# Kernel optimization log

Measured on AMD Instinct MI355X. Metric: run time of the kernel, lower is better.

## Reference

```python
import jax, jax.numpy as jnp
import numpy as np

BATCH_SIZE_PER_IM = 512
FG_FRACTION = 0.25
FG_THRESH = 0.5
BG_THRESH_HI = 0.5
BG_THRESH_LO = 0.0
MAX_FG = int(FG_FRACTION * BATCH_SIZE_PER_IM)  # 128


def _rand_boxes(key, shape):
    a = jax.random.uniform(key, shape + (4,), dtype=jnp.float32)
    ymin = jnp.minimum(a[..., 0], a[..., 2])
    ymax = jnp.maximum(a[..., 0], a[..., 2]) + 1e-3
    xmin = jnp.minimum(a[..., 1], a[..., 3])
    xmax = jnp.maximum(a[..., 1], a[..., 3]) + 1e-3
    return jnp.stack([ymin, xmin, ymax, xmax], axis=-1)


def setup_inputs() -> dict:
    key = jax.random.key(0)
    k1, k2, k3, k4 = jax.random.split(key, 4)
    B, N, G = 32, 8192, 128
    boxes = _rand_boxes(k1, (B, N))
    gt_boxes = _rand_boxes(k2, (B, G))
    gt_labels = jax.random.randint(k3, (B, G), 0, 91, dtype=jnp.int32)
    noise = jax.random.uniform(k4, (B, N + G), dtype=jnp.float32)
    return {"boxes": boxes, "gt_boxes": gt_boxes, "gt_labels": gt_labels, "noise": noise}


def _bbox_overlap(boxes, gt_boxes):
    # boxes: [B, M, 4], gt_boxes: [B, G, 4], layout (ymin, xmin, ymax, xmax)
    b_ymin, b_xmin, b_ymax, b_xmax = [boxes[..., i:i + 1] for i in range(4)]  # [B,M,1]
    g_ymin, g_xmin, g_ymax, g_xmax = [gt_boxes[..., i][:, None, :] for i in range(4)]  # [B,1,G]
    i_ymin = jnp.maximum(b_ymin, g_ymin)
    i_xmin = jnp.maximum(b_xmin, g_xmin)
    i_ymax = jnp.minimum(b_ymax, g_ymax)
    i_xmax = jnp.minimum(b_xmax, g_xmax)
    i_area = jnp.maximum(i_ymax - i_ymin, 0.0) * jnp.maximum(i_xmax - i_xmin, 0.0)  # [B,M,G]
    b_area = (b_ymax - b_ymin) * (b_xmax - b_xmin)           # [B,M,1]
    g_area = (g_ymax - g_ymin) * (g_xmax - g_xmin)           # [B,1,G]
    iou = i_area / (b_area + g_area - i_area)
    # padded gt boxes (filled with -1) get IoU = -1
    padding = jnp.logical_and(i_ymin < 0, i_xmin < 0)
    return jnp.where(padding, -1.0, iou)


def reference(boxes, gt_boxes, gt_labels, noise):
    boxes = jax.lax.stop_gradient(boxes)
    all_boxes = jnp.concatenate([boxes, gt_boxes], axis=1)        # [B, M=N+G, 4]
    iou = _bbox_overlap(all_boxes, gt_boxes)                      # [B, M, G]
    max_ov = jnp.max(iou, axis=2)                                 # [B, M]
    p2l = jnp.argmax(iou, axis=2).astype(jnp.int32)               # [B, M]
    box_t = jnp.take_along_axis(gt_boxes, p2l[..., None], axis=1)  # [B, M, 4]
    cls_t = jnp.take_along_axis(gt_labels, p2l, axis=1)           # [B, M]
    pos = max_ov > FG_THRESH
    neg = jnp.logical_and(max_ov >= BG_THRESH_LO, max_ov < BG_THRESH_HI)
    cls_t = jnp.where(neg, 0, cls_t)
    box_t = jnp.where(neg[..., None], 0.0, box_t)
    p2l = jnp.where(neg, 0, p2l)
    # --- balanced fg/bg subsampling (random scores provided in `noise`) ---
    pos_score = jnp.where(pos, noise, -1.0)
    kth = jax.lax.top_k(pos_score, MAX_FG)[0][:, -1:]             # [B,1] threshold
    sel_pos = jnp.logical_and(pos, pos_score >= kth)              # at most MAX_FG fg
    # selected fg get priority band 2+, bg band [0,1), rest -1
    combined = jnp.where(sel_pos, 2.0 + noise, jnp.where(neg, noise, -1.0))
    _, idx = jax.lax.top_k(combined, BATCH_SIZE_PER_IM)           # [B, K]
    rois = jnp.take_along_axis(all_boxes, idx[..., None], axis=1)      # [B, K, 4]
    sample_box_t = jnp.take_along_axis(box_t, idx[..., None], axis=1)  # [B, K, 4]
    sample_cls_t = jnp.take_along_axis(cls_t, idx, axis=1)             # [B, K]
    sample_p2l = jnp.take_along_axis(p2l, idx, axis=1)                 # [B, K]
    return sample_box_t, sample_cls_t, rois, sample_p2l
```

## Files before the change

### kernel.cpp

```cpp
#include <hip/hip_runtime.h>
#include <stdint.h>

#define BATCH 32
#define NBOX 8192
#define NGT 128
#define M (NBOX + NGT)
#define K_OUT 512
#define MAX_FG 128
#define C_CAP 256
#define S_CAP 256
#define U_CAP 1024

__device__ __forceinline__ unsigned int bkt1024(float ns) {
    unsigned int u = (unsigned int)(ns * 16777216.0f) >> 14;
    return u > 1023u ? 1023u : u;
}

__global__ __launch_bounds__(256) void iou_kernel(
    const float* __restrict__ boxes,
    const float* __restrict__ gt_boxes,
    unsigned short* __restrict__ packed)
{
    const int BPB = (M + 255) / 256;
    const int b = blockIdx.x / BPB;
    const int m = (blockIdx.x % BPB) * 256 + threadIdx.x;

    __shared__ float4 sgt[NGT];
    __shared__ float  sgarea[NGT];
    if (threadIdx.x < NGT) {
        float4 g = ((const float4*)gt_boxes)[b * NGT + threadIdx.x];
        sgt[threadIdx.x] = g;
        sgarea[threadIdx.x] = __fmul_rn(__fsub_rn(g.z, g.x), __fsub_rn(g.w, g.y));
    }
    __syncthreads();
    if (m >= M) return;

    float4 bb = (m < NBOX) ? ((const float4*)boxes)[b * NBOX + m]
                           : ((const float4*)gt_boxes)[b * NGT + (m - NBOX)];
    float b_area = __fmul_rn(__fsub_rn(bb.z, bb.x), __fsub_rn(bb.w, bb.y));

    float best = -1e30f;
    int bidx = 0;
    #pragma unroll 4
    for (int g = 0; g < NGT; ++g) {
        float4 gg = sgt[g];
        float iymin = fmaxf(bb.x, gg.x);
        float ixmin = fmaxf(bb.y, gg.y);
        float iymax = fminf(bb.z, gg.z);
        float ixmax = fminf(bb.w, gg.w);
        float ia  = __fmul_rn(fmaxf(__fsub_rn(iymax, iymin), 0.0f),
                              fmaxf(__fsub_rn(ixmax, ixmin), 0.0f));
        float den = __fsub_rn(__fadd_rn(b_area, sgarea[g]), ia);
        float iou = __fdiv_rn(ia, den);
        if (iou > best) { best = iou; bidx = g; }
    }
    bool pos = best > 0.5f;
    bool neg = (best >= 0.0f) && (best < 0.5f);
    packed[b * M + m] = (unsigned short)(bidx | (neg ? 256 : 0) | (pos ? 512 : 0));
}

__global__ __launch_bounds__(1024) void select_kernel(
    const float* __restrict__ boxes,
    const float* __restrict__ gt_boxes,
    const int*   __restrict__ gt_labels,
    const float* __restrict__ noise,
    const unsigned short* __restrict__ packed,
    float* __restrict__ out)
{
    const int b = blockIdx.x;
    const int tid = threadIdx.x;

    __shared__ float sh_ns[M];
    __shared__ unsigned int hist[1024];
    __shared__ unsigned int hist2[1024];
    __shared__ unsigned char posmask[M / 8];
    __shared__ unsigned char negmask[M / 8];
    __shared__ float4 sgt[NGT];
    __shared__ int slab[NGT];
    __shared__ float C[C_CAP];
    __shared__ unsigned short slist[S_CAP];
    __shared__ unsigned int ukey[U_CAP];
    __shared__ unsigned short um[U_CAP];
    __shared__ unsigned int sh_Bp, sh_needp, sh_cc, sh_n1a, sh_B, sh_cnt, sh_kth;

    float* out_bt  = out;
    float* out_cls = out + BATCH * K_OUT * 4;
    float* out_roi = out + BATCH * K_OUT * 5;
    float* out_p2l = out + BATCH * K_OUT * 9;

    hist[tid] = 0;
    hist2[tid] = 0;
    if (tid == 0) { sh_cc = 0; sh_n1a = 0; sh_B = 0; sh_cnt = 0; sh_kth = 0xBF800000u; }
    if (tid < NGT) {
        sgt[tid]  = ((const float4*)gt_boxes)[b * NGT + tid];
        slab[tid] = gt_labels[b * NGT + tid];
    }
    __syncthreads();

    {
        const uint4*  pk4 = (const uint4*)(packed + (size_t)b * M);
        const float4* ns4 = (const float4*)(noise + (size_t)b * M);
        for (int c = tid; c < M / 8; c += 1024) {
            uint4 pv = pk4[c];
            float4 n0 = ns4[2 * c], n1v = ns4[2 * c + 1];
            ((float4*)sh_ns)[2 * c] = n0;
            ((float4*)sh_ns)[2 * c + 1] = n1v;
            unsigned short e[8];
            e[0] = (unsigned short)(pv.x & 0xFFFF); e[1] = (unsigned short)(pv.x >> 16);
            e[2] = (unsigned short)(pv.y & 0xFFFF); e[3] = (unsigned short)(pv.y >> 16);
            e[4] = (unsigned short)(pv.z & 0xFFFF); e[5] = (unsigned short)(pv.z >> 16);
            e[6] = (unsigned short)(pv.w & 0xFFFF); e[7] = (unsigned short)(pv.w >> 16);
            float f[8] = {n0.x, n0.y, n0.z, n0.w, n1v.x, n1v.y, n1v.z, n1v.w};
            unsigned int pb = 0, nb = 0;
            #pragma unroll
            for (int k = 0; k < 8; ++k) {
                if (e[k] & 512) {
                    pb |= (1u << k);
                    atomicAdd(&hist2[bkt1024(f[k])], 1u);
                } else if (e[k] & 256) {
                    nb |= (1u << k);
                    atomicAdd(&hist[bkt1024(f[k])], 1u);
                }
            }
            posmask[c] = (unsigned char)pb;
            negmask[c] = (unsigned char)nb;
        }
    }
    __syncthreads();

    {
        const int wv = tid >> 6, ln = tid & 63;
        if (wv < 2) {
            unsigned int* H = wv ? hist2 : hist;
            unsigned int s[16];
            #pragma unroll
            for (int k = 0; k < 16; ++k) {
                unsigned int v = H[k * 64 + ln];
                #pragma unroll
                for (int off = 1; off < 64; off <<= 1) {
                    unsigned int o = __shfl_down(v, off, 64);
                    if (ln + off < 64) v += o;
                }
                s[k] = v;
            }
            unsigned int after = 0;
            #pragma unroll
            for (int k = 15; k >= 0; --k) {
                unsigned int tot = __shfl(s[k], 0, 64);
                H[k * 64 + ln] = s[k] + after;
                after += tot;
            }
        }
    }
    __syncthreads();
    const unsigned int nneg = hist[0];
    const unsigned int npos = hist2[0];

    if (npos >= MAX_FG) {
        {
            unsigned int S  = hist2[tid];
            unsigned int Sn = (tid < 1023) ? hist2[tid + 1] : 0;
            if (S >= MAX_FG && Sn < MAX_FG) { sh_Bp = tid; sh_needp = MAX_FG - Sn; }
        }
        __syncthreads();
        const unsigned int Bp = sh_Bp, needp = sh_needp;
        for (int c = tid; c < M / 8; c += 1024) {
            unsigned int pb = posmask[c];
            while (pb) {
                int k = __ffs(pb) - 1; pb &= pb - 1;
                float v = sh_ns[c * 8 + k];
                if (bkt1024(v) == Bp) {
                    unsigned int slot = atomicAdd(&sh_cc, 1u);
                    if (slot < C_CAP) C[slot] = v;
                }
            }
        }
        __syncthreads();
        {
            unsigned int cc = min(sh_cc, (unsigned int)C_CAP);
            if (tid < (int)cc) {
                float my = C[tid];
                unsigned int g = 0, e = 0;
                for (unsigned int j = 0; j < cc; ++j) {
                    float v = C[j];
                    g += (v > my) ? 1u : 0u;
                    e += (v == my) ? 1u : 0u;
                }
                if (g < needp && g + e >= needp) sh_kth = __float_as_uint(my);
            }
        }
        __syncthreads();
    }
    const float kthf = __uint_as_float(sh_kth);

    for (int c = tid; c < M / 8; c += 1024) {
        unsigned int pb = posmask[c];
        while (pb) {
            int k = __ffs(pb) - 1; pb &= pb - 1;
            int m = c * 8 + k;
            if (sh_ns[m] >= kthf) {
                unsigned int slot = atomicAdd(&sh_n1a, 1u);
                if (slot < S_CAP) slist[slot] = (unsigned short)m;
            }
        }
    }
    __syncthreads();
    const unsigned int n1 = min(sh_n1a, (unsigned int)S_CAP);
    const unsigned int k2 = K_OUT - n1;
    const bool enough_neg = (nneg >= k2);

    if (enough_neg) {
        unsigned int S  = hist[tid];
        unsigned int Sn = (tid < 1023) ? hist[tid + 1] : 0;
        if (S >= k2 && Sn < k2) sh_B = tid;
    }
    if (tid < (int)n1) {
        int mi = slist[tid];
        float nsi = sh_ns[mi];
        float ci = __fadd_rn(2.0f, nsi);
        unsigned int r = 0;
        for (unsigned int j = 0; j < n1; ++j) {
            int mj = slist[j];
            float cj = __fadd_rn(2.0f, sh_ns[mj]);
            if (cj > ci || (cj == ci && mj < mi)) ++r;
        }
        int pkv = packed[(size_t)b * M + mi];
        int lbl = pkv & 127;
        float4 roi = (mi < NBOX) ? ((const float4*)boxes)[b * NBOX + mi]
                                 : sgt[mi - NBOX];
        ((float4*)out_bt)[b * K_OUT + r] = sgt[lbl];
        out_cls[b * K_OUT + r] = (float)slab[lbl];
        ((float4*)out_roi)[b * K_OUT + r] = roi;
        out_p2l[b * K_OUT + r] = (float)lbl;
    }
    __syncthreads();
    const unsigned int B1 = sh_B;

    for (int c = tid; c < M / 8; c += 1024) {
        unsigned int nb = negmask[c];
        while (nb) {
            int k = __ffs(nb) - 1; nb &= nb - 1;
            int m = c * 8 + k;
            float v = sh_ns[m];
            if (bkt1024(v) >= B1) {
                unsigned int slot = atomicAdd(&sh_cnt, 1u);
                if (slot < U_CAP) {
                    ukey[slot] = __float_as_uint(v);
                    um[slot]   = (unsigned short)m;
                }
            }
        }
    }
    __syncthreads();

    const unsigned int q = min(sh_cnt, (unsigned int)U_CAP);
    for (unsigned int i = tid; i < q; i += 1024) {
        unsigned int ki = ukey[i];
        unsigned short mi = um[i];
        unsigned int r = 0;
        for (unsigned int j = 0; j < q; ++j) {
            unsigned int kj = ukey[j];
            if (kj > ki || (kj == ki && um[j] < mi)) ++r;
        }
        if (r < k2) {
            float4 roi = (mi < NBOX) ? ((const float4*)boxes)[b * NBOX + mi]
                                     : sgt[mi - NBOX];
            unsigned int gr = n1 + r;
            ((float4*)out_bt)[b * K_OUT + gr] = make_float4(0.f, 0.f, 0.f, 0.f);
            out_cls[b * K_OUT + gr] = 0.0f;
            ((float4*)out_roi)[b * K_OUT + gr] = roi;
            out_p2l[b * K_OUT + gr] = 0.0f;
        }
    }

    if (!enough_neg) {
        __syncthreads();
        const unsigned int k3 = k2 - nneg;
        for (int m = tid; m < M; m += 1024) {
            if (((posmask[m >> 3] >> (m & 7)) & 1) && sh_ns[m] < kthf) {
                unsigned int r = 0;
                for (int m2 = 0; m2 < m; ++m2)
                    if (((posmask[m2 >> 3] >> (m2 & 7)) & 1) && sh_ns[m2] < kthf) ++r;
                if (r < k3) {
                    int pkv = packed[(size_t)b * M + m];
                    int lbl = pkv & 127;
                    float4 roi = (m < NBOX) ? ((const float4*)boxes)[b * NBOX + m]
                                            : sgt[m - NBOX];
                    unsigned int gr = n1 + nneg + r;
                    ((float4*)out_bt)[b * K_OUT + gr] = sgt[lbl];
                    out_cls[b * K_OUT + gr] = (float)slab[lbl];
                    ((float4*)out_roi)[b * K_OUT + gr] = roi;
                    out_p2l[b * K_OUT + gr] = (float)lbl;
                }
            }
        }
    }
}

extern "C" void kernel_launch(void* const* d_in, const int* in_sizes, int n_in,
                              void* d_out, int out_size, void* d_ws, size_t ws_size,
                              hipStream_t stream) {
    const float* boxes     = (const float*)d_in[0];
    const float* gt_boxes  = (const float*)d_in[1];
    const int*   gt_labels = (const int*)d_in[2];
    const float* noise     = (const float*)d_in[3];
    unsigned short* packed = (unsigned short*)d_ws;
    float* out = (float*)d_out;

    const int BPB = (M + 255) / 256;
    iou_kernel<<<BATCH * BPB, 256, 0, stream>>>(boxes, gt_boxes, packed);
    select_kernel<<<BATCH, 1024, 0, stream>>>(boxes, gt_boxes, gt_labels, noise,
                                              packed, out);
}
```

Baseline: 116.6 us.

## Skip exact IoU division via threshold test, two boxes per thread, refine near ties

Each thread now handles two proposal boxes so every shared-memory GT load is reused twice. The per-pair exact division is replaced by a multiply-compare against half the denominator, and only candidates above 0.5 get an approximate reciprocal. The top two scores are tracked so that near-ties fall back to an exact rescan, and a final exact division recomputes the IoU for the winner. Boxes with no candidate are marked negative without their argmax index, which relies on that index being discarded for negatives (and on the inputs having no padded GT boxes).

```diff
diff --git a/kernel.cpp b/kernel.cpp
--- a/kernel.cpp
+++ b/kernel.cpp
@@ -21,42 +21,92 @@
     const float* __restrict__ gt_boxes,
     unsigned short* __restrict__ packed)
 {
-    const int BPB = (M + 255) / 256;
+    const int BPB = (M + 511) / 512;
     const int b = blockIdx.x / BPB;
-    const int m = (blockIdx.x % BPB) * 256 + threadIdx.x;
+    const int base = (blockIdx.x % BPB) * 512;
 
     __shared__ float4 sgt[NGT];
-    __shared__ float  sgarea[NGT];
+    __shared__ float  sga[NGT];
     if (threadIdx.x < NGT) {
         float4 g = ((const float4*)gt_boxes)[b * NGT + threadIdx.x];
         sgt[threadIdx.x] = g;
-        sgarea[threadIdx.x] = __fmul_rn(__fsub_rn(g.z, g.x), __fsub_rn(g.w, g.y));
-    }
-    __syncthreads();
-    if (m >= M) return;
-
-    float4 bb = (m < NBOX) ? ((const float4*)boxes)[b * NBOX + m]
-                           : ((const float4*)gt_boxes)[b * NGT + (m - NBOX)];
-    float b_area = __fmul_rn(__fsub_rn(bb.z, bb.x), __fsub_rn(bb.w, bb.y));
-
-    float best = -1e30f;
-    int bidx = 0;
+        sga[threadIdx.x] = __fmul_rn(__fsub_rn(g.z, g.x), __fsub_rn(g.w, g.y));
+    }
+    __syncthreads();
+
+    const int r0 = base + threadIdx.x;
+    const int r1 = r0 + 256;
+
+    float4 A  = make_float4(0.f, 0.f, 0.f, 0.f);
+    float4 Bx = make_float4(0.f, 0.f, 0.f, 0.f);
+    if (r0 < M) A  = (r0 < NBOX) ? ((const float4*)boxes)[b * NBOX + r0] : sgt[r0 - NBOX];
+    if (r1 < M) Bx = (r1 < NBOX) ? ((const float4*)boxes)[b * NBOX + r1] : sgt[r1 - NBOX];
+    const float areaA = __fmul_rn(__fsub_rn(A.z, A.x),  __fsub_rn(A.w, A.y));
+    const float areaB = __fmul_rn(__fsub_rn(Bx.z, Bx.x), __fsub_rn(Bx.w, Bx.y));
+
+    float best0 = 0.f, sec0 = 0.f; int i0 = 0;
+    float best1 = 0.f, sec1 = 0.f; int i1 = 0;
+
     #pragma unroll 4
     for (int g = 0; g < NGT; ++g) {
         float4 gg = sgt[g];
-        float iymin = fmaxf(bb.x, gg.x);
-        float ixmin = fmaxf(bb.y, gg.y);
-        float iymax = fminf(bb.z, gg.z);
-        float ixmax = fminf(bb.w, gg.w);
-        float ia  = __fmul_rn(fmaxf(__fsub_rn(iymax, iymin), 0.0f),
-                              fmaxf(__fsub_rn(ixmax, ixmin), 0.0f));
-        float den = __fsub_rn(__fadd_rn(b_area, sgarea[g]), ia);
-        float iou = __fdiv_rn(ia, den);
-        if (iou > best) { best = iou; bidx = g; }
-    }
-    bool pos = best > 0.5f;
-    bool neg = (best >= 0.0f) && (best < 0.5f);
-    packed[b * M + m] = (unsigned short)(bidx | (neg ? 256 : 0) | (pos ? 512 : 0));
+        float ga = sga[g];
+        {
+            float dy = __fsub_rn(fminf(A.z, gg.z), fmaxf(A.x, gg.x));
+            float dx = __fsub_rn(fminf(A.w, gg.w), fmaxf(A.y, gg.y));
+            float ia = __fmul_rn(fmaxf(dy, 0.f), fmaxf(dx, 0.f));
+            float den = __fsub_rn(__fadd_rn(areaA, ga), ia);
+            if (ia > __fmul_rn(0.5f, den)) {
+                float q = __fmul_rn(ia, __builtin_amdgcn_rcpf(den));
+                if (q > best0)      { sec0 = best0; best0 = q; i0 = g; }
+                else if (q > sec0)  { sec0 = q; }
+            }
+        }
+        {
+            float dy = __fsub_rn(fminf(Bx.z, gg.z), fmaxf(Bx.x, gg.x));
+            float dx = __fsub_rn(fminf(Bx.w, gg.w), fmaxf(Bx.y, gg.y));
+            float ia = __fmul_rn(fmaxf(dy, 0.f), fmaxf(dx, 0.f));
+            float den = __fsub_rn(__fadd_rn(areaB, ga), ia);
+            if (ia > __fmul_rn(0.5f, den)) {
+                float q = __fmul_rn(ia, __builtin_amdgcn_rcpf(den));
+                if (q > best1)      { sec1 = best1; best1 = q; i1 = g; }
+                else if (q > sec1)  { sec1 = q; }
+            }
+        }
+    }
+
+    auto finalize = [&](float4 bb, float barea, float best, float sec,
+                        int bi) -> unsigned short {
+        if (best == 0.f) return (unsigned short)256;
+        bool flag = __fsub_rn(best, sec) <= __fmul_rn(best, 1.9073486e-6f);
+        int bidx; float q;
+        if (!flag) {
+            bidx = bi;
+            float4 gg = sgt[bidx];
+            float dy = __fsub_rn(fminf(bb.z, gg.z), fmaxf(bb.x, gg.x));
+            float dx = __fsub_rn(fminf(bb.w, gg.w), fmaxf(bb.y, gg.y));
+            float ia = __fmul_rn(fmaxf(dy, 0.f), fmaxf(dx, 0.f));
+            float den = __fsub_rn(__fadd_rn(barea, sga[bidx]), ia);
+            q = __fdiv_rn(ia, den);
+        } else {
+            float bq = -1e30f; bidx = 0;
+            for (int g = 0; g < NGT; ++g) {
+                float4 gg = sgt[g];
+                float dy = __fsub_rn(fminf(bb.z, gg.z), fmaxf(bb.x, gg.x));
+                float dx = __fsub_rn(fminf(bb.w, gg.w), fmaxf(bb.y, gg.y));
+                float ia = __fmul_rn(fmaxf(dy, 0.f), fmaxf(dx, 0.f));
+                float den = __fsub_rn(__fadd_rn(barea, sga[g]), ia);
+                float qg = __fdiv_rn(ia, den);
+                if (qg > bq) { bq = qg; bidx = g; }
+            }
+            q = bq;
+        }
+        bool pos = q > 0.5f;
+        return (unsigned short)(pos ? (bidx | 512) : 256);
+    };
+
+    if (r0 < M) packed[b * M + r0] = finalize(A,  areaA, best0, sec0, i0);
+    if (r1 < M) packed[b * M + r1] = finalize(Bx, areaB, best1, sec1, i1);
 }
 
 __global__ __launch_bounds__(1024) void select_kernel(
@@ -307,7 +357,7 @@
     unsigned short* packed = (unsigned short*)d_ws;
     float* out = (float*)d_out;
 
-    const int BPB = (M + 255) / 256;
+    const int BPB = (M + 511) / 512;
     iou_kernel<<<BATCH * BPB, 256, 0, stream>>>(boxes, gt_boxes, packed);
     select_kernel<<<BATCH, 1024, 0, stream>>>(boxes, gt_boxes, gt_labels, noise,
                                               packed, out);
```

Result: no change. 118.4 us (+1.6%).

## Register-block IoU over four boxes per thread with division-free threshold filtering

Applied to the files above, without the earlier changes.

Each thread now handles four proposal boxes, reading gt boxes straight from global/cache instead of LDS, and computing IoU only when intersection exceeds half the union, using a fast reciprocal. A best/second-best tracker detects near-ties, and those cases fall back to an exact recomputation with correctly rounded division, so argmax and the threshold flags should match the original. This removes the per-pair exact division and the shared-memory staging, at the cost of more registers and a divergent fallback path. Neg is now implied for every non-positive box, which assumes no padded gt boxes (IoU of -1) appear in the inputs.

```diff
diff --git a/kernel.cpp b/kernel.cpp
--- a/kernel.cpp
+++ b/kernel.cpp
@@ -21,42 +21,87 @@
     const float* __restrict__ gt_boxes,
     unsigned short* __restrict__ packed)
 {
-    const int BPB = (M + 255) / 256;
+    const int BPB = 9;
     const int b = blockIdx.x / BPB;
-    const int m = (blockIdx.x % BPB) * 256 + threadIdx.x;
-
-    __shared__ float4 sgt[NGT];
-    __shared__ float  sgarea[NGT];
-    if (threadIdx.x < NGT) {
-        float4 g = ((const float4*)gt_boxes)[b * NGT + threadIdx.x];
-        sgt[threadIdx.x] = g;
-        sgarea[threadIdx.x] = __fmul_rn(__fsub_rn(g.z, g.x), __fsub_rn(g.w, g.y));
-    }
-    __syncthreads();
-    if (m >= M) return;
-
-    float4 bb = (m < NBOX) ? ((const float4*)boxes)[b * NBOX + m]
-                           : ((const float4*)gt_boxes)[b * NGT + (m - NBOX)];
-    float b_area = __fmul_rn(__fsub_rn(bb.z, bb.x), __fsub_rn(bb.w, bb.y));
-
-    float best = -1e30f;
-    int bidx = 0;
+    const int base = (blockIdx.x % BPB) * 1024 + threadIdx.x;
+
+    const float4* __restrict__ gt = ((const float4*)gt_boxes) + b * NGT;
+    const float4* __restrict__ bx = ((const float4*)boxes) + b * NBOX;
+
+    float4 R[4];
+    float  area[4];
+    bool   valid[4];
+    #pragma unroll
+    for (int k = 0; k < 4; ++k) {
+        int r = base + k * 256;
+        valid[k] = (r < M);
+        float4 v = make_float4(0.f, 0.f, 0.f, 0.f);
+        if (valid[k]) v = (r < NBOX) ? bx[r] : gt[r - NBOX];
+        R[k] = v;
+        area[k] = __fmul_rn(__fsub_rn(v.z, v.x), __fsub_rn(v.w, v.y));
+    }
+
+    float best[4] = {0.f, 0.f, 0.f, 0.f};
+    float sec[4]  = {0.f, 0.f, 0.f, 0.f};
+    int   bi[4]   = {0, 0, 0, 0};
+
     #pragma unroll 4
     for (int g = 0; g < NGT; ++g) {
-        float4 gg = sgt[g];
-        float iymin = fmaxf(bb.x, gg.x);
-        float ixmin = fmaxf(bb.y, gg.y);
-        float iymax = fminf(bb.z, gg.z);
-        float ixmax = fminf(bb.w, gg.w);
-        float ia  = __fmul_rn(fmaxf(__fsub_rn(iymax, iymin), 0.0f),
-                              fmaxf(__fsub_rn(ixmax, ixmin), 0.0f));
-        float den = __fsub_rn(__fadd_rn(b_area, sgarea[g]), ia);
-        float iou = __fdiv_rn(ia, den);
-        if (iou > best) { best = iou; bidx = g; }
-    }
-    bool pos = best > 0.5f;
-    bool neg = (best >= 0.0f) && (best < 0.5f);
-    packed[b * M + m] = (unsigned short)(bidx | (neg ? 256 : 0) | (pos ? 512 : 0));
+        float4 gg = gt[g];
+        float ga = __fmul_rn(__fsub_rn(gg.z, gg.x), __fsub_rn(gg.w, gg.y));
+        #pragma unroll
+        for (int k = 0; k < 4; ++k) {
+            float dy = __fsub_rn(fminf(R[k].z, gg.z), fmaxf(R[k].x, gg.x));
+            float dx = __fsub_rn(fminf(R[k].w, gg.w), fmaxf(R[k].y, gg.y));
+            float ia = __fmul_rn(fmaxf(dy, 0.f), fmaxf(dx, 0.f));
+            float den = __fsub_rn(__fadd_rn(area[k], ga), ia);
+            if (ia > __fmul_rn(0.5f, den)) {
+                float q = __fmul_rn(ia, __builtin_amdgcn_rcpf(den));
+                if (q > best[k])      { sec[k] = best[k]; best[k] = q; bi[k] = g; }
+                else if (q > sec[k])  { sec[k] = q; }
+            }
+        }
+    }
+
+    #pragma unroll
+    for (int k = 0; k < 4; ++k) {
+        if (!valid[k]) continue;
+        int r = base + k * 256;
+        unsigned short pk;
+        if (best[k] == 0.f) {
+            pk = (unsigned short)256;
+        } else {
+            bool flag = __fsub_rn(best[k], sec[k]) <=
+                        __fmul_rn(best[k], 1.9073486e-6f);
+            int bidx; float q;
+            if (!flag) {
+                bidx = bi[k];
+                float4 gg = gt[bidx];
+                float dy = __fsub_rn(fminf(R[k].z, gg.z), fmaxf(R[k].x, gg.x));
+                float dx = __fsub_rn(fminf(R[k].w, gg.w), fmaxf(R[k].y, gg.y));
+                float ia = __fmul_rn(fmaxf(dy, 0.f), fmaxf(dx, 0.f));
+                float ga = __fmul_rn(__fsub_rn(gg.z, gg.x), __fsub_rn(gg.w, gg.y));
+                float den = __fsub_rn(__fadd_rn(area[k], ga), ia);
+                q = __fdiv_rn(ia, den);
+            } else {
+                float bq = -1e30f; bidx = 0;
+                for (int g = 0; g < NGT; ++g) {
+                    float4 gg = gt[g];
+                    float dy = __fsub_rn(fminf(R[k].z, gg.z), fmaxf(R[k].x, gg.x));
+                    float dx = __fsub_rn(fminf(R[k].w, gg.w), fmaxf(R[k].y, gg.y));
+                    float ia = __fmul_rn(fmaxf(dy, 0.f), fmaxf(dx, 0.f));
+                    float ga = __fmul_rn(__fsub_rn(gg.z, gg.x), __fsub_rn(gg.w, gg.y));
+                    float den = __fsub_rn(__fadd_rn(area[k], ga), ia);
+                    float qg = __fdiv_rn(ia, den);
+                    if (qg > bq) { bq = qg; bidx = g; }
+                }
+                q = bq;
+            }
+            bool pos = q > 0.5f;
+            pk = (unsigned short)(pos ? (bidx | 512) : 256);
+        }
+        packed[b * M + r] = pk;
+    }
 }
 
 __global__ __launch_bounds__(1024) void select_kernel(
@@ -307,8 +352,7 @@
     unsigned short* packed = (unsigned short*)d_ws;
     float* out = (float*)d_out;
 
-    const int BPB = (M + 255) / 256;
-    iou_kernel<<<BATCH * BPB, 256, 0, stream>>>(boxes, gt_boxes, packed);
+    iou_kernel<<<BATCH * 9, 256, 0, stream>>>(boxes, gt_boxes, packed);
     select_kernel<<<BATCH, 1024, 0, stream>>>(boxes, gt_boxes, gt_labels, noise,
                                               packed, out);
 }
```

After: 143.2 us. +22.8%, slower.

## Replace per-pair IoU division with threshold test and refine argmax for candidates

Applied to the files above, without the earlier changes.

The IoU kernel no longer divides for every box/gt pair. It checks `ia - 0.5*den > 0` to flag rows that may be foreground and writes a magic marker for them; all other rows are marked background directly. A new wave-per-strip kernel finds the flagged rows by ballot and computes the exact IoU argmax over the 128 gts with one lane per gt pair and a shuffle reduction. This removes most of the expensive IEEE divisions, at the cost of an extra kernel launch and possible rounding differences at the 0.5 boundary.

```diff
diff --git a/kernel.cpp b/kernel.cpp
--- a/kernel.cpp
+++ b/kernel.cpp
@@ -10,6 +10,7 @@
 #define C_CAP 256
 #define S_CAP 256
 #define U_CAP 1024
+#define CAND_MAGIC 0xFFFFu
 
 __device__ __forceinline__ unsigned int bkt1024(float ns) {
     unsigned int u = (unsigned int)(ns * 16777216.0f) >> 14;
@@ -24,39 +25,85 @@
     const int BPB = (M + 255) / 256;
     const int b = blockIdx.x / BPB;
     const int m = (blockIdx.x % BPB) * 256 + threadIdx.x;
-
-    __shared__ float4 sgt[NGT];
-    __shared__ float  sgarea[NGT];
-    if (threadIdx.x < NGT) {
-        float4 g = ((const float4*)gt_boxes)[b * NGT + threadIdx.x];
-        sgt[threadIdx.x] = g;
-        sgarea[threadIdx.x] = __fmul_rn(__fsub_rn(g.z, g.x), __fsub_rn(g.w, g.y));
-    }
-    __syncthreads();
     if (m >= M) return;
 
+    const float4* __restrict__ gt = ((const float4*)gt_boxes) + b * NGT;
+
     float4 bb = (m < NBOX) ? ((const float4*)boxes)[b * NBOX + m]
-                           : ((const float4*)gt_boxes)[b * NGT + (m - NBOX)];
-    float b_area = __fmul_rn(__fsub_rn(bb.z, bb.x), __fsub_rn(bb.w, bb.y));
-
-    float best = -1e30f;
-    int bidx = 0;
+                           : gt[m - NBOX];
+    const float barea = __fmul_rn(__fsub_rn(bb.z, bb.x), __fsub_rn(bb.w, bb.y));
+
+    float acc = -1.0f;
     #pragma unroll 4
     for (int g = 0; g < NGT; ++g) {
-        float4 gg = sgt[g];
-        float iymin = fmaxf(bb.x, gg.x);
-        float ixmin = fmaxf(bb.y, gg.y);
-        float iymax = fminf(bb.z, gg.z);
-        float ixmax = fminf(bb.w, gg.w);
-        float ia  = __fmul_rn(fmaxf(__fsub_rn(iymax, iymin), 0.0f),
-                              fmaxf(__fsub_rn(ixmax, ixmin), 0.0f));
-        float den = __fsub_rn(__fadd_rn(b_area, sgarea[g]), ia);
-        float iou = __fdiv_rn(ia, den);
-        if (iou > best) { best = iou; bidx = g; }
-    }
-    bool pos = best > 0.5f;
-    bool neg = (best >= 0.0f) && (best < 0.5f);
-    packed[b * M + m] = (unsigned short)(bidx | (neg ? 256 : 0) | (pos ? 512 : 0));
+        float4 gg = gt[g];
+        float ga = __fmul_rn(__fsub_rn(gg.z, gg.x), __fsub_rn(gg.w, gg.y));
+        float dy = __fsub_rn(fminf(bb.z, gg.z), fmaxf(bb.x, gg.x));
+        float dx = __fsub_rn(fminf(bb.w, gg.w), fmaxf(bb.y, gg.y));
+        float ia = __fmul_rn(fmaxf(dy, 0.f), fmaxf(dx, 0.f));
+        float den = __fsub_rn(__fadd_rn(barea, ga), ia);
+        acc = fmaxf(acc, __fsub_rn(ia, __fmul_rn(0.5f, den)));
+    }
+    packed[b * M + m] = (acc > 0.f) ? (unsigned short)CAND_MAGIC
+                                    : (unsigned short)256;
+}
+
+__global__ __launch_bounds__(256) void argmax_kernel(
+    const float* __restrict__ boxes,
+    const float* __restrict__ gt_boxes,
+    unsigned short* __restrict__ packed)
+{
+    const int lane = threadIdx.x & 63;
+    const int gw = blockIdx.x * 4 + (threadIdx.x >> 6);
+    const int NSTRIP = BATCH * (M / 64);
+
+    for (int strip = gw; strip < NSTRIP; strip += gridDim.x * 4) {
+        const int b = strip / (M / 64);
+        const int row0 = (strip % (M / 64)) * 64;
+        const float4* __restrict__ gt = ((const float4*)gt_boxes) + b * NGT;
+
+        unsigned short pk = packed[(size_t)b * M + row0 + lane];
+        unsigned long long mask = __ballot(pk == CAND_MAGIC);
+        while (mask) {
+            int bit = __ffsll((long long)mask) - 1; mask &= mask - 1;
+            int row = row0 + bit;
+            float4 bb = (row < NBOX) ? ((const float4*)boxes)[b * NBOX + row]
+                                     : gt[row - NBOX];
+            float barea = __fmul_rn(__fsub_rn(bb.z, bb.x), __fsub_rn(bb.w, bb.y));
+
+            int g0 = lane, g1 = lane + 64;
+            float q0, q1;
+            {
+                float4 gg = gt[g0];
+                float ga = __fmul_rn(__fsub_rn(gg.z, gg.x), __fsub_rn(gg.w, gg.y));
+                float dy = __fsub_rn(fminf(bb.z, gg.z), fmaxf(bb.x, gg.x));
+                float dx = __fsub_rn(fminf(bb.w, gg.w), fmaxf(bb.y, gg.y));
+                float ia = __fmul_rn(fmaxf(dy, 0.f), fmaxf(dx, 0.f));
+                float den = __fsub_rn(__fadd_rn(barea, ga), ia);
+                q0 = __fdiv_rn(ia, den);
+            }
+            {
+                float4 gg = gt[g1];
+                float ga = __fmul_rn(__fsub_rn(gg.z, gg.x), __fsub_rn(gg.w, gg.y));
+                float dy = __fsub_rn(fminf(bb.z, gg.z), fmaxf(bb.x, gg.x));
+                float dx = __fsub_rn(fminf(bb.w, gg.w), fmaxf(bb.y, gg.y));
+                float ia = __fmul_rn(fmaxf(dy, 0.f), fmaxf(dx, 0.f));
+                float den = __fsub_rn(__fadd_rn(barea, ga), ia);
+                q1 = __fdiv_rn(ia, den);
+            }
+            float qv = q0; int qi = g0;
+            if (q1 > q0) { qv = q1; qi = g1; }
+            #pragma unroll
+            for (int off = 1; off < 64; off <<= 1) {
+                float ov = __shfl_xor(qv, off, 64);
+                int   oi = __shfl_xor(qi, off, 64);
+                if (ov > qv || (ov == qv && oi < qi)) { qv = ov; qi = oi; }
+            }
+            if (lane == 0)
+                packed[(size_t)b * M + row] =
+                    (qv > 0.5f) ? (unsigned short)(qi | 512) : (unsigned short)256;
+        }
+    }
 }
 
 __global__ __launch_bounds__(1024) void select_kernel(
@@ -309,6 +356,7 @@
 
     const int BPB = (M + 255) / 256;
     iou_kernel<<<BATCH * BPB, 256, 0, stream>>>(boxes, gt_boxes, packed);
+    argmax_kernel<<<520, 256, 0, stream>>>(boxes, gt_boxes, packed);
     select_kernel<<<BATCH, 1024, 0, stream>>>(boxes, gt_boxes, gt_labels, noise,
                                               packed, out);
 }
```

Measured after the change: 224.1 us. +92.2%, slower.
